# Kernel optimization log

Measured on AMD Instinct MI355X. Metric: run time of the kernel, lower is better.

## Reference

```python
import jax, jax.numpy as jnp
import numpy as np

B, T, K, N, D = 4, 1024, 3, 4, 64
TIME_SCALES = [1, 2, 4]  # sorted, scale 1 included; N = lcm = 4
PHASE = 1


def _build_routing_tables(phase):
    # PhaseTables._build_stream_head_maps, SHARED assignment, single phase
    stream_ids = np.arange(N)
    s2h = np.empty((K, N), dtype=np.int32)
    h2s = np.empty((K, N), dtype=np.int32)
    for k, s in enumerate(TIME_SCALES):
        alpha = N // s
        j = phase % s
        row = (stream_ids + alpha * j) % N
        s2h[k] = row
        inv = np.empty_like(row)
        inv[row] = stream_ids
        h2s[k] = inv
    return jnp.asarray(s2h), jnp.asarray(h2s)


def setup_inputs() -> dict:
    key = jax.random.key(0)
    kx, kw = jax.random.split(key)
    x = jax.random.normal(kx, (B, T, K, N, D), dtype=jnp.float32)
    # trunc_normal_init_ with std = 1/sqrt(in_dim); plain normal*std is a faithful stand-in
    Wqkv = jax.random.normal(kw, (K, N, D, 3 * D), dtype=jnp.float32) * (1.0 / D ** 0.5)
    s2h, h2s = _build_routing_tables(PHASE)
    return {"x": x, "Wqkv": Wqkv, "stream_to_head": s2h, "head_to_stream": h2s}


def _route_n(x_btkni, idx_kn):
    # out[b,t,k,n,i] = x[b,t,k,idx_kn[k,n],i]  (torch.gather along dim=3)
    k_idx = jnp.arange(K)[:, None]  # [K,1] broadcasts with idx_kn [K,N]
    return x_btkni[:, :, k_idx, idx_kn, :]


def _forward(x, Wqkv, stream_to_head, head_to_stream):
    # SLOT-scope SHARED projection: streams -> heads, grouped projection, heads -> streams
    x_head = _route_n(x, head_to_stream)                       # [B,T,K,N,D]
    qkv_head = jnp.einsum('btkni,knio->btkno', x_head, Wqkv)   # [B,T,K,N,3D]
    qkv = _route_n(qkv_head, stream_to_head)                   # stream order

    # AttentionAdapter (SDPA, causal, dropout_p=0, no rope)
    H = K * N
    qkv = qkv.reshape(B, T, H, 3, D)
    q = qkv[..., 0, :].transpose(0, 2, 1, 3)  # [B,H,T,D]
    k = qkv[..., 1, :].transpose(0, 2, 1, 3)
    v = qkv[..., 2, :].transpose(0, 2, 1, 3)
    scale = 1.0 / jnp.sqrt(jnp.asarray(D, dtype=q.dtype))
    scores = jnp.einsum('bhtd,bhsd->bhts', q, k) * scale       # [B,H,T,T]
    causal = jnp.tril(jnp.ones((T, T), dtype=bool))
    scores = jnp.where(causal, scores, jnp.finfo(scores.dtype).min)
    probs = jax.nn.softmax(scores, axis=-1)
    out_bhtd = jnp.einsum('bhts,bhsd->bhtd', probs, v)          # [B,H,T,D]
    # reshape to [B,K,N,T,D] then permute -> [B,T,K,N,D]
    out = out_bhtd.reshape(B, K, N, T, D).transpose(0, 3, 1, 2, 4)
    return out


def reference(x, Wqkv, stream_to_head, head_to_stream):
    return _forward(x, Wqkv, stream_to_head, head_to_stream)
```

## Files before the change

kernel.cpp:

```cpp
#include <hip/hip_runtime.h>

using f32x4 = __attribute__((ext_vector_type(4))) float;
using s16x8 = __attribute__((ext_vector_type(8))) short;

constexpr int B = 4, T = 1024, H = 12, D = 64;
constexpr int LD = 72;

__device__ __forceinline__ short f2bf(float f) {
    unsigned u = __float_as_uint(f);
    u = (u + 0x7fffu + ((u >> 16) & 1u)) >> 16;
    return (short)u;
}
__device__ __forceinline__ short f2bf_trunc(float f) {
    return (short)(__float_as_uint(f) >> 16);
}

__global__ __launch_bounds__(256) void wprep_kernel(
    const float* __restrict__ W, const int* __restrict__ s2h,
    short* __restrict__ wt_ws)
{
    __shared__ float tile[64][68];
    const int h = blockIdx.x, ot = blockIdx.y;
    const int kk = h >> 2, m = s2h[h];
    const float* Wp = W + (size_t)(kk * 4 + m) * D * 192 + ot * 64;
    const float qs = (ot == 0) ? 0.125f * 1.44269504f : 1.0f;
    const int tid = threadIdx.x;
    for (int e = tid; e < 1024; e += 256) {
        const int i = e >> 4, o4 = e & 15;
        float4 v = *reinterpret_cast<const float4*>(Wp + (size_t)i * 192 + o4 * 4);
        tile[i][o4 * 4 + 0] = v.x * qs;
        tile[i][o4 * 4 + 1] = v.y * qs;
        tile[i][o4 * 4 + 2] = v.z * qs;
        tile[i][o4 * 4 + 3] = v.w * qs;
    }
    __syncthreads();
    short* op = wt_ws + (size_t)h * 192 * 64 + (size_t)ot * 64 * 64;
    for (int e = tid; e < 1024; e += 256) {
        const int o = e >> 4, i4 = e & 15;
        short4 s = make_short4(f2bf(tile[i4 * 4 + 0][o]), f2bf(tile[i4 * 4 + 1][o]),
                               f2bf(tile[i4 * 4 + 2][o]), f2bf(tile[i4 * 4 + 3][o]));
        *reinterpret_cast<short4*>(op + o * 64 + i4 * 4) = s;
    }
}

__global__ __launch_bounds__(256) void proj_kernel(
    const float* __restrict__ x, const short* __restrict__ wt_ws,
    short* __restrict__ qw, short* __restrict__ kw, short* __restrict__ vt)
{
    __shared__ short buf[64 * LD + 192 * LD];
    short* ax = buf;
    short* wt = buf + 64 * LD;
    short* eq = buf;
    short* ek = buf + 64 * LD;
    short* ev = buf + 128 * LD;

    const int h = blockIdx.y;
    const int tid = threadIdx.x;
    const int t0g = blockIdx.x * 64;
    const int b = t0g / T, t0 = t0g % T;
    const int bh = b * H + h;
    const int ct = t0 >> 6;

    const float* xp = x + ((size_t)(b * T + t0) * H + h) * D;
    for (int e4 = tid; e4 < 64 * 16; e4 += 256) {
        const int row = e4 >> 4, i4 = e4 & 15;
        float4 v = *reinterpret_cast<const float4*>(xp + (size_t)row * H * D + i4 * 4);
        *reinterpret_cast<short4*>(&ax[row * LD + i4 * 4]) =
            make_short4(f2bf(v.x), f2bf(v.y), f2bf(v.z), f2bf(v.w));
    }
    const short* wtp = wt_ws + (size_t)h * 192 * 64;
    for (int e8 = tid; e8 < 192 * 8; e8 += 256) {
        const int row = e8 >> 3, c8 = e8 & 7;
        *reinterpret_cast<uint4*>(&wt[row * LD + c8 * 8]) =
            *reinterpret_cast<const uint4*>(wtp + (size_t)row * 64 + c8 * 8);
    }
    __syncthreads();

    const int wv = tid >> 6, lane = tid & 63, quad = lane >> 4, c = lane & 15;
    s16x8 af[4][2];
    #pragma unroll
    for (int mb = 0; mb < 4; ++mb)
        #pragma unroll
        for (int ks = 0; ks < 2; ++ks)
            af[mb][ks] = *reinterpret_cast<const s16x8*>(
                &ax[(mb * 16 + c) * LD + ks * 32 + quad * 8]);

    f32x4 acc[4][3];
    #pragma unroll
    for (int mb = 0; mb < 4; ++mb)
        #pragma unroll
        for (int nb = 0; nb < 3; ++nb)
            acc[mb][nb] = (f32x4){0.f, 0.f, 0.f, 0.f};

    #pragma unroll
    for (int nb = 0; nb < 3; ++nb) {
        const int o16 = nb * 4 + wv;
        #pragma unroll
        for (int ks = 0; ks < 2; ++ks) {
            s16x8 bf = *reinterpret_cast<const s16x8*>(
                &wt[(o16 * 16 + c) * LD + ks * 32 + quad * 8]);
            #pragma unroll
            for (int mb = 0; mb < 4; ++mb)
                acc[mb][nb] = __builtin_amdgcn_mfma_f32_16x16x32_bf16(
                    af[mb][ks], bf, acc[mb][nb], 0, 0, 0);
        }
    }
    __syncthreads();

    const int d = wv * 16 + c;
    #pragma unroll
    for (int mb = 0; mb < 4; ++mb) {
        #pragma unroll
        for (int reg = 0; reg < 4; ++reg) {
            const int tl = mb * 16 + quad * 4 + reg;
            eq[tl * LD + d] = f2bf(acc[mb][0][reg]);
            ek[tl * LD + d] = f2bf(acc[mb][1][reg]);
        }
        short4 sv = make_short4(f2bf(acc[mb][2][0]), f2bf(acc[mb][2][1]),
                                f2bf(acc[mb][2][2]), f2bf(acc[mb][2][3]));
        *reinterpret_cast<short4*>(&ev[d * LD + mb * 16 + quad * 4]) = sv;
    }
    __syncthreads();

    for (int e = tid; e < 512; e += 256) {
        const int r = e >> 3, seg = e & 7;
        uint4 vq = *reinterpret_cast<const uint4*>(&eq[r * LD + seg * 8]);
        uint4 vk = *reinterpret_cast<const uint4*>(&ek[r * LD + seg * 8]);
        uint4 vv = *reinterpret_cast<const uint4*>(&ev[r * LD + seg * 8]);
        *reinterpret_cast<uint4*>(qw + ((size_t)bh * T + t0 + r) * 64 + seg * 8) = vq;
        *reinterpret_cast<uint4*>(kw + ((size_t)bh * T + t0 + r) * 64 + seg * 8) = vk;
        *reinterpret_cast<uint4*>(vt + (((size_t)bh * 16 + ct) * 64 + r) * 64 + seg * 8) = vv;
    }
}

__global__ __launch_bounds__(256) void attn_kernel(
    const short* __restrict__ qw, const short* __restrict__ kw,
    const short* __restrict__ vt, float* __restrict__ out)
{
    __shared__ short lk[64 * LD];
    __shared__ short lv[64 * LD];
    __shared__ short lp[4][16 * LD];

    const int idx = blockIdx.x;
    const int bh = idx % 48;
    const int qt = ((idx / 48) * 11) & 15;
    const int b = bh / H, h = bh % H;
    const int tid = threadIdx.x, wv = tid >> 6, lane = tid & 63;
    const int quad = lane >> 4, c = lane & 15;
    const int r0 = qt * 64;

    s16x8 qf[2];
    {
        const short* qp = qw + ((size_t)bh * T + r0 + wv * 16 + c) * 64;
        qf[0] = *reinterpret_cast<const s16x8*>(qp + quad * 8);
        qf[1] = *reinterpret_cast<const s16x8*>(qp + 32 + quad * 8);
    }

    f32x4 oacc[4];
    #pragma unroll
    for (int cb = 0; cb < 4; ++cb) oacc[cb] = (f32x4){0.f, 0.f, 0.f, 0.f};
    float l_run = 0.f;
    short* lpw = lp[wv];

    for (int ch = 0; ch <= qt; ++ch) {
        __syncthreads();
        const short* kp = kw + ((size_t)bh * T + ch * 64) * 64;
        const short* vp = vt + (((size_t)bh * 16 + ch) * 64) * 64;
        for (int e8 = tid; e8 < 512; e8 += 256) {
            const int r = e8 >> 3, c8 = e8 & 7;
            *reinterpret_cast<uint4*>(&lk[r * LD + c8 * 8]) =
                *reinterpret_cast<const uint4*>(kp + r * 64 + c8 * 8);
            *reinterpret_cast<uint4*>(&lv[r * LD + c8 * 8]) =
                *reinterpret_cast<const uint4*>(vp + r * 64 + c8 * 8);
        }
        __syncthreads();

        const bool diag = (ch == qt);
        float lsum = 0.f;
        #pragma unroll
        for (int st = 0; st < 4; ++st) {
            s16x8 a0 = *reinterpret_cast<const s16x8*>(
                &lk[(st * 16 + c) * LD + quad * 8]);
            s16x8 a1 = *reinterpret_cast<const s16x8*>(
                &lk[(st * 16 + c) * LD + 32 + quad * 8]);
            f32x4 sacc = (f32x4){0.f, 0.f, 0.f, 0.f};
            sacc = __builtin_amdgcn_mfma_f32_16x16x32_bf16(a0, qf[0], sacc, 0, 0, 0);
            sacc = __builtin_amdgcn_mfma_f32_16x16x32_bf16(a1, qf[1], sacc, 0, 0, 0);
            if (diag) {
                #pragma unroll
                for (int reg = 0; reg < 4; ++reg)
                    if (st * 16 + quad * 4 + reg > wv * 16 + c) sacc[reg] = -1e30f;
            }
            float p0 = __builtin_amdgcn_exp2f(sacc[0] - 8.0f);
            float p1 = __builtin_amdgcn_exp2f(sacc[1] - 8.0f);
            float p2 = __builtin_amdgcn_exp2f(sacc[2] - 8.0f);
            float p3 = __builtin_amdgcn_exp2f(sacc[3] - 8.0f);
            lsum += (p0 + p1) + (p2 + p3);
            *reinterpret_cast<short4*>(&lpw[c * LD + st * 16 + quad * 4]) =
                make_short4(f2bf_trunc(p0), f2bf_trunc(p1),
                            f2bf_trunc(p2), f2bf_trunc(p3));
        }
        lsum += __shfl_xor(lsum, 16);
        lsum += __shfl_xor(lsum, 32);
        l_run += lsum;

        #pragma unroll
        for (int ks2 = 0; ks2 < 2; ++ks2) {
            s16x8 pa = *reinterpret_cast<const s16x8*>(
                &lpw[c * LD + ks2 * 32 + quad * 8]);
            #pragma unroll
            for (int cb = 0; cb < 4; ++cb) {
                s16x8 bf = *reinterpret_cast<const s16x8*>(
                    &lv[(cb * 16 + c) * LD + ks2 * 32 + quad * 8]);
                oacc[cb] = __builtin_amdgcn_mfma_f32_16x16x32_bf16(
                    pa, bf, oacc[cb], 0, 0, 0);
            }
        }
    }

    float linv[4];
    #pragma unroll
    for (int reg = 0; reg < 4; ++reg)
        linv[reg] = 1.0f / __shfl(l_run, quad * 4 + reg);

    #pragma unroll
    for (int cb = 0; cb < 4; ++cb)
        #pragma unroll
        for (int reg = 0; reg < 4; ++reg) {
            const int t = r0 + wv * 16 + quad * 4 + reg;
            out[((size_t)(b * T + t) * H + h) * D + cb * 16 + c] =
                oacc[cb][reg] * linv[reg];
        }
}

extern "C" void kernel_launch(void* const* d_in, const int* in_sizes, int n_in,
                              void* d_out, int out_size, void* d_ws, size_t ws_size,
                              hipStream_t stream) {
    const float* x   = (const float*)d_in[0];
    const float* W   = (const float*)d_in[1];
    const int*   s2h = (const int*)d_in[2];
    float* out = (float*)d_out;

    short* wt_ws = (short*)d_ws;
    short* qw    = wt_ws + (size_t)12 * 192 * 64;
    short* kw    = qw + (size_t)B * H * T * D;
    short* vt    = kw + (size_t)B * H * T * D;

    wprep_kernel<<<dim3(H, 3), 256, 0, stream>>>(W, s2h, wt_ws);
    proj_kernel<<<dim3(B * T / 64, H), 256, 0, stream>>>(x, wt_ws, qw, kw, vt);
    attn_kernel<<<dim3((T / 64) * (B * H)), 256, 0, stream>>>(qw, kw, vt, out);
}
```

Measured before the change: 108.3 us.

## Double-buffer K tiles via register prefetch and load V fragments directly from global

The attention loop now prefetches the next K chunk into registers while computing the current one, storing it into a double-buffered LDS array, which removes one of the two block barriers per chunk. The V operand fragments are read straight from global memory into registers instead of being staged through LDS, because each wave uses them in MFMA layout. This cuts LDS traffic and synchronisation. In exchange it raises register pressure and issues uncoalesced-ish global loads of V that are each read redundantly by all four waves.

Result: slower. 117.6 us (+8.5%).

```diff
diff --git a/kernel.cpp b/kernel.cpp
--- a/kernel.cpp
+++ b/kernel.cpp
@@ -137,8 +137,7 @@
     const short* __restrict__ qw, const short* __restrict__ kw,
     const short* __restrict__ vt, float* __restrict__ out)
 {
-    __shared__ short lk[64 * LD];
-    __shared__ short lv[64 * LD];
+    __shared__ short lk[2][64 * LD];
     __shared__ short lp[4][16 * LD];
 
     const int idx = blockIdx.x;
@@ -162,27 +161,49 @@
     float l_run = 0.f;
     short* lpw = lp[wv];
 
+    const short* kbase = kw + (size_t)bh * T * 64;
+    const short* vbase = vt + (size_t)bh * 16 * 64 * 64;
+
+    const int srow = tid >> 3, sseg = tid & 7;
+
+    uint4 kreg0, kreg1;
+    {
+        const short* kp = kbase;
+        kreg0 = *reinterpret_cast<const uint4*>(kp + (size_t)srow * 64 + sseg * 8);
+        kreg1 = *reinterpret_cast<const uint4*>(kp + (size_t)(srow + 32) * 64 + sseg * 8);
+    }
+
     for (int ch = 0; ch <= qt; ++ch) {
+        short* lkc = lk[ch & 1];
+        *reinterpret_cast<uint4*>(&lkc[srow * LD + sseg * 8]) = kreg0;
+        *reinterpret_cast<uint4*>(&lkc[(srow + 32) * LD + sseg * 8]) = kreg1;
         __syncthreads();
-        const short* kp = kw + ((size_t)bh * T + ch * 64) * 64;
-        const short* vp = vt + (((size_t)bh * 16 + ch) * 64) * 64;
-        for (int e8 = tid; e8 < 512; e8 += 256) {
-            const int r = e8 >> 3, c8 = e8 & 7;
-            *reinterpret_cast<uint4*>(&lk[r * LD + c8 * 8]) =
-                *reinterpret_cast<const uint4*>(kp + r * 64 + c8 * 8);
-            *reinterpret_cast<uint4*>(&lv[r * LD + c8 * 8]) =
-                *reinterpret_cast<const uint4*>(vp + r * 64 + c8 * 8);
-        }
-        __syncthreads();
+
+        if (ch < qt) {
+            const short* kp = kbase + (size_t)(ch + 1) * 64 * 64;
+            kreg0 = *reinterpret_cast<const uint4*>(kp + (size_t)srow * 64 + sseg * 8);
+            kreg1 = *reinterpret_cast<const uint4*>(kp + (size_t)(srow + 32) * 64 + sseg * 8);
+        }
+
+        s16x8 vf[2][4];
+        {
+            const short* vp = vbase + (size_t)ch * 64 * 64;
+            #pragma unroll
+            for (int ks2 = 0; ks2 < 2; ++ks2)
+                #pragma unroll
+                for (int cb = 0; cb < 4; ++cb)
+                    vf[ks2][cb] = *reinterpret_cast<const s16x8*>(
+                        vp + (size_t)(cb * 16 + c) * 64 + ks2 * 32 + quad * 8);
+        }
 
         const bool diag = (ch == qt);
         float lsum = 0.f;
         #pragma unroll
         for (int st = 0; st < 4; ++st) {
             s16x8 a0 = *reinterpret_cast<const s16x8*>(
-                &lk[(st * 16 + c) * LD + quad * 8]);
+                &lkc[(st * 16 + c) * LD + quad * 8]);
             s16x8 a1 = *reinterpret_cast<const s16x8*>(
-                &lk[(st * 16 + c) * LD + 32 + quad * 8]);
+                &lkc[(st * 16 + c) * LD + 32 + quad * 8]);
             f32x4 sacc = (f32x4){0.f, 0.f, 0.f, 0.f};
             sacc = __builtin_amdgcn_mfma_f32_16x16x32_bf16(a0, qf[0], sacc, 0, 0, 0);
             sacc = __builtin_amdgcn_mfma_f32_16x16x32_bf16(a1, qf[1], sacc, 0, 0, 0);
@@ -209,12 +230,9 @@
             s16x8 pa = *reinterpret_cast<const s16x8*>(
                 &lpw[c * LD + ks2 * 32 + quad * 8]);
             #pragma unroll
-            for (int cb = 0; cb < 4; ++cb) {
-                s16x8 bf = *reinterpret_cast<const s16x8*>(
-                    &lv[(cb * 16 + c) * LD + ks2 * 32 + quad * 8]);
+            for (int cb = 0; cb < 4; ++cb)
                 oacc[cb] = __builtin_amdgcn_mfma_f32_16x16x32_bf16(
-                    pa, bf, oacc[cb], 0, 0, 0);
-            }
+                    pa, vf[ks2][cb], oacc[cb], 0, 0, 0);
         }
     }
 
```

## Process 32 query rows per wave in attention with 128-thread blocks

Applied to the files above, without the earlier changes.

The attention kernel now uses 2 waves per block, and each wave handles two 16-row query tiles instead of one. Every K and V fragment read from LDS is reused for two MFMAs, which halves LDS fragment traffic per unit of compute and adds instruction-level parallelism. The cost is roughly doubled accumulator and Q register use per thread, fewer threads sharing the cooperative K/V tile loads, and fewer waves per block to hide latency.

Result: slower. 120.8 us (+11.5%).

```diff
diff --git a/kernel.cpp b/kernel.cpp
--- a/kernel.cpp
+++ b/kernel.cpp
@@ -133,13 +133,13 @@
     }
 }
 
-__global__ __launch_bounds__(256) void attn_kernel(
+__global__ __launch_bounds__(128) void attn_kernel(
     const short* __restrict__ qw, const short* __restrict__ kw,
     const short* __restrict__ vt, float* __restrict__ out)
 {
     __shared__ short lk[64 * LD];
     __shared__ short lv[64 * LD];
-    __shared__ short lp[4][16 * LD];
+    __shared__ short lp[2][32 * LD];
 
     const int idx = blockIdx.x;
     const int bh = idx % 48;
@@ -149,24 +149,27 @@
     const int quad = lane >> 4, c = lane & 15;
     const int r0 = qt * 64;
 
-    s16x8 qf[2];
-    {
-        const short* qp = qw + ((size_t)bh * T + r0 + wv * 16 + c) * 64;
-        qf[0] = *reinterpret_cast<const s16x8*>(qp + quad * 8);
-        qf[1] = *reinterpret_cast<const s16x8*>(qp + 32 + quad * 8);
-    }
-
-    f32x4 oacc[4];
-    #pragma unroll
-    for (int cb = 0; cb < 4; ++cb) oacc[cb] = (f32x4){0.f, 0.f, 0.f, 0.f};
-    float l_run = 0.f;
+    s16x8 qf[2][2];
+    #pragma unroll
+    for (int rt = 0; rt < 2; ++rt) {
+        const short* qp = qw + ((size_t)bh * T + r0 + wv * 32 + rt * 16 + c) * 64;
+        qf[rt][0] = *reinterpret_cast<const s16x8*>(qp + quad * 8);
+        qf[rt][1] = *reinterpret_cast<const s16x8*>(qp + 32 + quad * 8);
+    }
+
+    f32x4 oacc[2][4];
+    #pragma unroll
+    for (int rt = 0; rt < 2; ++rt)
+        #pragma unroll
+        for (int cb = 0; cb < 4; ++cb) oacc[rt][cb] = (f32x4){0.f, 0.f, 0.f, 0.f};
+    float l_run[2] = {0.f, 0.f};
     short* lpw = lp[wv];
 
     for (int ch = 0; ch <= qt; ++ch) {
         __syncthreads();
         const short* kp = kw + ((size_t)bh * T + ch * 64) * 64;
         const short* vp = vt + (((size_t)bh * 16 + ch) * 64) * 64;
-        for (int e8 = tid; e8 < 512; e8 += 256) {
+        for (int e8 = tid; e8 < 512; e8 += 128) {
             const int r = e8 >> 3, c8 = e8 & 7;
             *reinterpret_cast<uint4*>(&lk[r * LD + c8 * 8]) =
                 *reinterpret_cast<const uint4*>(kp + r * 64 + c8 * 8);
@@ -176,61 +179,75 @@
         __syncthreads();
 
         const bool diag = (ch == qt);
-        float lsum = 0.f;
+        float lsum[2] = {0.f, 0.f};
         #pragma unroll
         for (int st = 0; st < 4; ++st) {
             s16x8 a0 = *reinterpret_cast<const s16x8*>(
                 &lk[(st * 16 + c) * LD + quad * 8]);
             s16x8 a1 = *reinterpret_cast<const s16x8*>(
                 &lk[(st * 16 + c) * LD + 32 + quad * 8]);
-            f32x4 sacc = (f32x4){0.f, 0.f, 0.f, 0.f};
-            sacc = __builtin_amdgcn_mfma_f32_16x16x32_bf16(a0, qf[0], sacc, 0, 0, 0);
-            sacc = __builtin_amdgcn_mfma_f32_16x16x32_bf16(a1, qf[1], sacc, 0, 0, 0);
-            if (diag) {
-                #pragma unroll
-                for (int reg = 0; reg < 4; ++reg)
-                    if (st * 16 + quad * 4 + reg > wv * 16 + c) sacc[reg] = -1e30f;
+            #pragma unroll
+            for (int rt = 0; rt < 2; ++rt) {
+                f32x4 sacc = (f32x4){0.f, 0.f, 0.f, 0.f};
+                sacc = __builtin_amdgcn_mfma_f32_16x16x32_bf16(a0, qf[rt][0], sacc, 0, 0, 0);
+                sacc = __builtin_amdgcn_mfma_f32_16x16x32_bf16(a1, qf[rt][1], sacc, 0, 0, 0);
+                if (diag) {
+                    const int qloc = wv * 32 + rt * 16 + c;
+                    #pragma unroll
+                    for (int reg = 0; reg < 4; ++reg)
+                        if (st * 16 + quad * 4 + reg > qloc) sacc[reg] = -1e30f;
+                }
+                float p0 = __builtin_amdgcn_exp2f(sacc[0] - 8.0f);
+                float p1 = __builtin_amdgcn_exp2f(sacc[1] - 8.0f);
+                float p2 = __builtin_amdgcn_exp2f(sacc[2] - 8.0f);
+                float p3 = __builtin_amdgcn_exp2f(sacc[3] - 8.0f);
+                lsum[rt] += (p0 + p1) + (p2 + p3);
+                *reinterpret_cast<short4*>(&lpw[(rt * 16 + c) * LD + st * 16 + quad * 4]) =
+                    make_short4(f2bf_trunc(p0), f2bf_trunc(p1),
+                                f2bf_trunc(p2), f2bf_trunc(p3));
             }
-            float p0 = __builtin_amdgcn_exp2f(sacc[0] - 8.0f);
-            float p1 = __builtin_amdgcn_exp2f(sacc[1] - 8.0f);
-            float p2 = __builtin_amdgcn_exp2f(sacc[2] - 8.0f);
-            float p3 = __builtin_amdgcn_exp2f(sacc[3] - 8.0f);
-            lsum += (p0 + p1) + (p2 + p3);
-            *reinterpret_cast<short4*>(&lpw[c * LD + st * 16 + quad * 4]) =
-                make_short4(f2bf_trunc(p0), f2bf_trunc(p1),
-                            f2bf_trunc(p2), f2bf_trunc(p3));
-        }
-        lsum += __shfl_xor(lsum, 16);
-        lsum += __shfl_xor(lsum, 32);
-        l_run += lsum;
+        }
+        #pragma unroll
+        for (int rt = 0; rt < 2; ++rt) {
+            float ls = lsum[rt];
+            ls += __shfl_xor(ls, 16);
+            ls += __shfl_xor(ls, 32);
+            l_run[rt] += ls;
+        }
 
         #pragma unroll
         for (int ks2 = 0; ks2 < 2; ++ks2) {
-            s16x8 pa = *reinterpret_cast<const s16x8*>(
+            s16x8 pa0 = *reinterpret_cast<const s16x8*>(
                 &lpw[c * LD + ks2 * 32 + quad * 8]);
+            s16x8 pa1 = *reinterpret_cast<const s16x8*>(
+                &lpw[(16 + c) * LD + ks2 * 32 + quad * 8]);
             #pragma unroll
             for (int cb = 0; cb < 4; ++cb) {
                 s16x8 bf = *reinterpret_cast<const s16x8*>(
                     &lv[(cb * 16 + c) * LD + ks2 * 32 + quad * 8]);
-                oacc[cb] = __builtin_amdgcn_mfma_f32_16x16x32_bf16(
-                    pa, bf, oacc[cb], 0, 0, 0);
+                oacc[0][cb] = __builtin_amdgcn_mfma_f32_16x16x32_bf16(pa0, bf, oacc[0][cb], 0, 0, 0);
+                oacc[1][cb] = __builtin_amdgcn_mfma_f32_16x16x32_bf16(pa1, bf, oacc[1][cb], 0, 0, 0);
             }
         }
     }
 
-    float linv[4];
-    #pragma unroll
-    for (int reg = 0; reg < 4; ++reg)
-        linv[reg] = 1.0f / __shfl(l_run, quad * 4 + reg);
-
-    #pragma unroll
-    for (int cb = 0; cb < 4; ++cb)
-        #pragma unroll
-        for (int reg = 0; reg < 4; ++reg) {
-            const int t = r0 + wv * 16 + quad * 4 + reg;
-            out[((size_t)(b * T + t) * H + h) * D + cb * 16 + c] =
-                oacc[cb][reg] * linv[reg];
-        }
+    float linv[2][4];
+    #pragma unroll
+    for (int rt = 0; rt < 2; ++rt)
+        #pragma unroll
+        for (int reg = 0; reg < 4; ++reg)
+            linv[rt][reg] = 1.0f / __shfl(l_run[rt], quad * 4 + reg);
+
+    #pragma unroll
+    for (int rt = 0; rt < 2; ++rt)
+        #pragma unroll
+        for (int cb = 0; cb < 4; ++cb)
+            #pragma unroll
+            for (int reg = 0; reg < 4; ++reg) {
+                const int t = r0 + wv * 32 + rt * 16 + quad * 4 + reg;
+                out[((size_t)(b * T + t) * H + h) * D + cb * 16 + c] =
+                    oacc[rt][cb][reg] * linv[rt][reg];
+            }
 }
 
 extern "C" void kernel_launch(void* const* d_in, const int* in_sizes, int n_in,
@@ -248,5 +265,5 @@
 
     wprep_kernel<<<dim3(H, 3), 256, 0, stream>>>(W, s2h, wt_ws);
     proj_kernel<<<dim3(B * T / 64, H), 256, 0, stream>>>(x, wt_ws, qw, kw, vt);
-    attn_kernel<<<dim3((T / 64) * (B * H)), 256, 0, stream>>>(qw, kw, vt, out);
-}
+    attn_kernel<<<dim3((T / 64) * (B * H)), 128, 0, stream>>>(qw, kw, vt, out);
+}
```

## Split long causal attention query tiles across two blocks and merge partials

Applied to the files above, without the earlier changes.

Query tiles 8-15, which have the most causal KV chunks, are split into two work units each. Every unit writes unnormalized partial outputs and row sums to workspace, and a new merge kernel adds the two halves and normalizes. A static table orders the units longest first to balance load across CUs and shorten the tail. The merge needs no max rescaling because the kernel uses no running max. The cost is an extra kernel launch plus workspace traffic for the partial results.

Result: faster. 103.0 us (-4.9%).

```diff
diff --git a/kernel.cpp b/kernel.cpp
--- a/kernel.cpp
+++ b/kernel.cpp
@@ -14,6 +14,14 @@
 __device__ __forceinline__ short f2bf_trunc(float f) {
     return (short)(__float_as_uint(f) >> 16);
 }
+
+__device__ const int4 UNITS[24] = {
+    {15,0,7,14},{15,8,15,15},{14,7,14,13},{7,0,7,-1},
+    {14,0,6,12},{13,0,6,10},{13,7,13,11},{12,6,12,9},{6,0,6,-1},
+    {12,0,5,8},{11,0,5,6},{11,6,11,7},{10,5,10,5},{5,0,5,-1},
+    {10,0,4,4},{9,0,4,2},{9,5,9,3},{8,4,8,1},{4,0,4,-1},
+    {8,0,3,0},{3,0,3,-1},{2,0,2,-1},{1,0,1,-1},{0,0,0,-1}
+};
 
 __global__ __launch_bounds__(256) void wprep_kernel(
     const float* __restrict__ W, const int* __restrict__ s2h,
@@ -135,7 +143,8 @@
 
 __global__ __launch_bounds__(256) void attn_kernel(
     const short* __restrict__ qw, const short* __restrict__ kw,
-    const short* __restrict__ vt, float* __restrict__ out)
+    const short* __restrict__ vt, float* __restrict__ out,
+    float* __restrict__ po, float* __restrict__ pl)
 {
     __shared__ short lk[64 * LD];
     __shared__ short lv[64 * LD];
@@ -143,7 +152,8 @@
 
     const int idx = blockIdx.x;
     const int bh = idx % 48;
-    const int qt = ((idx / 48) * 11) & 15;
+    const int4 u = UNITS[idx / 48];
+    const int qt = u.x, ch0 = u.y, ch1 = u.z, slot = u.w;
     const int b = bh / H, h = bh % H;
     const int tid = threadIdx.x, wv = tid >> 6, lane = tid & 63;
     const int quad = lane >> 4, c = lane & 15;
@@ -162,7 +172,7 @@
     float l_run = 0.f;
     short* lpw = lp[wv];
 
-    for (int ch = 0; ch <= qt; ++ch) {
+    for (int ch = ch0; ch <= ch1; ++ch) {
         __syncthreads();
         const short* kp = kw + ((size_t)bh * T + ch * 64) * 64;
         const short* vp = vt + (((size_t)bh * 16 + ch) * 64) * 64;
@@ -218,19 +228,58 @@
         }
     }
 
-    float linv[4];
-    #pragma unroll
-    for (int reg = 0; reg < 4; ++reg)
-        linv[reg] = 1.0f / __shfl(l_run, quad * 4 + reg);
-
-    #pragma unroll
-    for (int cb = 0; cb < 4; ++cb)
-        #pragma unroll
-        for (int reg = 0; reg < 4; ++reg) {
-            const int t = r0 + wv * 16 + quad * 4 + reg;
-            out[((size_t)(b * T + t) * H + h) * D + cb * 16 + c] =
-                oacc[cb][reg] * linv[reg];
-        }
+    if (slot < 0) {
+        float linv[4];
+        #pragma unroll
+        for (int reg = 0; reg < 4; ++reg)
+            linv[reg] = 1.0f / __shfl(l_run, quad * 4 + reg);
+        #pragma unroll
+        for (int cb = 0; cb < 4; ++cb)
+            #pragma unroll
+            for (int reg = 0; reg < 4; ++reg) {
+                const int t = r0 + wv * 16 + quad * 4 + reg;
+                out[((size_t)(b * T + t) * H + h) * D + cb * 16 + c] =
+                    oacc[cb][reg] * linv[reg];
+            }
+    } else {
+        float* pob = po + (((size_t)bh * 16 + slot) * 64) * 64;
+        #pragma unroll
+        for (int cb = 0; cb < 4; ++cb)
+            #pragma unroll
+            for (int reg = 0; reg < 4; ++reg)
+                pob[(size_t)(wv * 16 + quad * 4 + reg) * 64 + cb * 16 + c] =
+                    oacc[cb][reg];
+        if (quad == 0)
+            pl[((size_t)bh * 16 + slot) * 64 + wv * 16 + c] = l_run;
+    }
+}
+
+__global__ __launch_bounds__(256) void merge_kernel(
+    const float* __restrict__ po, const float* __restrict__ pl,
+    float* __restrict__ out)
+{
+    const int m = blockIdx.x;
+    const int bh = m % 48, qi = m / 48;
+    const int b = bh / H, h = bh % H;
+    const int sa = qi * 2, sb = sa + 1;
+    const int tid = threadIdx.x;
+    const int r = tid >> 2, dseg = (tid & 3) * 16;
+
+    const float la = pl[((size_t)bh * 16 + sa) * 64 + r]
+                   + pl[((size_t)bh * 16 + sb) * 64 + r];
+    const float inv = 1.0f / la;
+    const float* pa = po + (((size_t)bh * 16 + sa) * 64 + r) * 64 + dseg;
+    const float* pb = po + (((size_t)bh * 16 + sb) * 64 + r) * 64 + dseg;
+    const int t = (qi + 8) * 64 + r;
+    float* op = out + ((size_t)(b * T + t) * H + h) * D + dseg;
+    #pragma unroll
+    for (int j = 0; j < 4; ++j) {
+        float4 va = *reinterpret_cast<const float4*>(pa + j * 4);
+        float4 vb = *reinterpret_cast<const float4*>(pb + j * 4);
+        float4 vo = make_float4((va.x + vb.x) * inv, (va.y + vb.y) * inv,
+                                (va.z + vb.z) * inv, (va.w + vb.w) * inv);
+        *reinterpret_cast<float4*>(op + j * 4) = vo;
+    }
 }
 
 extern "C" void kernel_launch(void* const* d_in, const int* in_sizes, int n_in,
@@ -245,8 +294,11 @@
     short* qw    = wt_ws + (size_t)12 * 192 * 64;
     short* kw    = qw + (size_t)B * H * T * D;
     short* vt    = kw + (size_t)B * H * T * D;
+    float* po    = (float*)(vt + (size_t)B * H * 16 * 64 * 64);
+    float* pl    = po + (size_t)B * H * 16 * 64 * 64;
 
     wprep_kernel<<<dim3(H, 3), 256, 0, stream>>>(W, s2h, wt_ws);
     proj_kernel<<<dim3(B * T / 64, H), 256, 0, stream>>>(x, wt_ws, qw, kw, vt);
-    attn_kernel<<<dim3((T / 64) * (B * H)), 256, 0, stream>>>(qw, kw, vt, out);
-}
+    attn_kernel<<<dim3(24 * 48), 256, 0, stream>>>(qw, kw, vt, out, po, pl);
+    merge_kernel<<<dim3(8 * 48), 256, 0, stream>>>(po, pl, out);
+}
```
